# Kernel tuning notes

Hardware: AMD Instinct MI355X
Metric: run time of the kernel (lower is better)

## Reference

```python
import jax, jax.numpy as jnp
import numpy as np

B, H, W = 1, 32, 32
C, G, K = 128, 4, 15
GC = C // G          # group channels = 32
K2 = K * K           # 225
RED = 4              # SE reduction
KHID = 32            # kernel_net hidden


def setup_inputs() -> dict:
    key = jax.random.key(0)
    ks = jax.random.split(key, 24)
    def n(k, shape, s=0.02):
        return jax.random.normal(k, shape, jnp.float32) * s
    inp = {
        'x': jax.random.normal(ks[0], (B, H, W, C), jnp.float32),
        # scalars (torch: raw_sigma init = softplus^{-1}(0.3), base_offset_scale = 0.1)
        'raw_sigma': jnp.asarray(float(np.log(np.expm1(0.3))), jnp.float32),
        'base_offset_scale': jnp.asarray(0.1, jnp.float32),
        # input/output projections
        'w_in': n(ks[1], (C, C)), 'b_in': jnp.zeros((C,), jnp.float32),
        'w_out': n(ks[2], (C, C)), 'b_out': jnp.zeros((C,), jnp.float32),
        # dw_conv: depthwise 3x3 (HWIO, I=1 per group) + pointwise 1x1
        'dw_k': n(ks[3], (3, 3, 1, C), 0.1), 'dw_b': jnp.zeros((C,), jnp.float32),
        'pw_w': n(ks[4], (C, C)), 'pw_b': jnp.zeros((C,), jnp.float32),
        # offset / mask nets (zero-init in torch; small random here to exercise gather)
        'off_w': n(ks[5], (C, G * K2 * 2), 0.01), 'off_b': n(ks[6], (G * K2 * 2,), 0.01),
        'msk_w': n(ks[7], (C, G * K2), 0.01), 'msk_b': n(ks[8], (G * K2,), 0.01),
        # kernel_net: 2 -> 32 -> 32 -> G*GC
        'k1_w': n(ks[9], (2, KHID), 0.3), 'k1_b': jnp.zeros((KHID,), jnp.float32),
        'k2_w': n(ks[10], (KHID, KHID), 0.2), 'k2_b': jnp.zeros((KHID,), jnp.float32),
        'k3_w': n(ks[11], (KHID, G * GC), 0.2), 'k3_b': jnp.zeros((G * GC,), jnp.float32),
        # SE block
        'se1_w': n(ks[12], (C, C // RED), 0.1), 'se1_b': jnp.zeros((C // RED,), jnp.float32),
        'se2_w': n(ks[13], (C // RED, C), 0.1), 'se2_b': jnp.zeros((C,), jnp.float32),
    }
    return inp


def reference(x, raw_sigma, base_offset_scale, w_in, b_in, w_out, b_out,
              dw_k, dw_b, pw_w, pw_b, off_w, off_b, msk_w, msk_b,
              k1_w, k1_b, k2_w, k2_b, k3_w, k3_b, se1_w, se1_b, se2_w, se2_b):
    # sigma (scalar path, biases=None)
    sigma = jnp.clip(jax.nn.softplus(raw_sigma), 0.001, 0.5)
    grid = jnp.linspace(-0.5, 0.5, K)

    x_proj = x @ w_in + b_in                                   # [B,H,W,C]

    # dw_conv: depthwise 3x3 -> SiLU -> 1x1
    y = jax.lax.conv_general_dilated(
        x, dw_k, (1, 1), 'SAME',
        dimension_numbers=('NHWC', 'HWIO', 'NHWC'),
        feature_group_count=C) + dw_b
    x_dw = jax.nn.silu(y) @ pw_w + pw_b                        # [B,H,W,C]

    # Gaussian envelope over kernel grid, normalized (scalar sigma -> shape [K,K])
    gh = grid[:, None]; gw = grid[None, :]
    env = jnp.exp(-(gh ** 2 + gw ** 2) / (2.0 * sigma ** 2))
    env = env / jnp.clip(env.sum(), 1e-8)                      # [K,K]

    # dynamic kernel weights from grid positions (*2); replicate torch's
    # contiguous view (K,K,G,gc) -> (G,K2,gc)
    pos = jnp.stack(jnp.meshgrid(grid, grid, indexing='ij'), -1).reshape(K2, 2) * 2.0
    h1 = jax.nn.silu(pos @ k1_w + k1_b)
    h2 = jax.nn.silu(h1 @ k2_w + k2_b)
    kw = (h2 @ k3_w + k3_b).reshape(K, K, G, GC).reshape(G, K2, GC)  # [G,K2,gc]

    offsets = (x_dw @ off_w + off_b).reshape(B, H, W, G, K2, 2) * base_offset_scale
    raw_mask = (x_dw @ msk_w + msk_b).reshape(B, H, W, G, K2) * env.reshape(1, 1, 1, 1, K2)
    attn = jnp.nan_to_num(jax.nn.softmax(raw_mask, axis=-1))   # [B,H,W,G,K2]

    # reference sampling grid (integer offsets -K//2..K//2)
    ref = jnp.linspace(-(K // 2), K // 2, K)
    ref_grid = jnp.stack(jnp.meshgrid(ref, ref, indexing='ij'), -1).reshape(K2, 2)
    pos_h = jnp.arange(H, dtype=jnp.float32).reshape(1, H, 1, 1, 1)
    pos_w = jnp.arange(W, dtype=jnp.float32).reshape(1, 1, W, 1, 1)

    abs_h = pos_h + ref_grid[:, 0].reshape(1, 1, 1, 1, K2) + offsets[..., 0]
    abs_w = pos_w + ref_grid[:, 1].reshape(1, 1, 1, 1, K2) + offsets[..., 1]
    ah = jnp.clip(abs_h, 0.0, H - 1); aw = jnp.clip(abs_w, 0.0, W - 1)
    hf = jnp.clip(ah.astype(jnp.int32), 0, H - 1)
    wf = jnp.clip(aw.astype(jnp.int32), 0, W - 1)
    hc = jnp.clip(hf + 1, 0, H - 1)
    wc = jnp.clip(wf + 1, 0, W - 1)
    hw = ah - hf.astype(jnp.float32)
    ww = aw - wf.astype(jnp.float32)
    valid = (~((abs_h < 0) | (abs_h > H - 1) | (abs_w < 0) | (abs_w > W - 1))).astype(jnp.float32)

    x_g = x_proj.reshape(B, H, W, G, GC)
    b_idx = jnp.arange(B).reshape(B, 1, 1, 1, 1)
    g_idx = jnp.arange(G).reshape(1, 1, 1, G, 1)
    def gather(hi, wi):
        return x_g[b_idx, hi, wi, g_idx]                       # [B,H,W,G,K2,gc]

    sampled = (gather(hf, wf) * ((1 - hw) * (1 - ww) * valid)[..., None]
             + gather(hf, wc) * ((1 - hw) * ww * valid)[..., None]
             + gather(hc, wf) * (hw * (1 - ww) * valid)[..., None]
             + gather(hc, wc) * (hw * ww * valid)[..., None])

    sampled = sampled * kw.reshape(1, 1, 1, G, K2, GC)
    out = jnp.einsum('bhwgkc,bhwgk->bhwgc', sampled, attn).reshape(B, H, W, C)

    # SE block (mask=None, bias=None)
    pooled = out.mean(axis=(1, 2), keepdims=True)
    scale = jax.nn.sigmoid(jax.nn.silu(pooled @ se1_w + se1_b) @ se2_w + se2_b)
    out = out * scale

    return out @ w_out + b_out
```

## Files before the change

kernel.cpp:

```cpp
#include <hip/hip_runtime.h>
#include <math.h>

constexpr int H = 32, W = 32, C = 128, G = 4, K = 15, K2 = 225, GC = 32;
constexpr int NPIX = H * W;
constexpr int NOFF = G * K2 * 2;
constexpr int NMSK = G * K2;
constexpr int NTOT = NOFF + NMSK;
constexpr int KHID = 32;

constexpr size_t WS_ENV    = 0;
constexpr size_t WS_KW     = 256;
constexpr size_t WS_SCALE  = 29184;
constexpr size_t WS_PART   = 29312;
constexpr size_t WS_XPROJ  = 33792;
constexpr size_t WS_XDW    = 164864;
constexpr size_t WS_OUTPRE = 295936;
constexpr size_t WS_OFFS   = 427008;
constexpr size_t WS_MASK   = 2270208;

__device__ __forceinline__ float sigmoidf_(float v) { return 1.f / (1.f + expf(-v)); }
__device__ __forceinline__ float siluf_(float v)    { return v / (1.f + expf(-v)); }

__global__ void env_kernel(const float* __restrict__ raw_sigma, float* __restrict__ ws) {
    __shared__ float red[256];
    int tid = threadIdx.x;
    float xs = raw_sigma[0];
    float sp = fmaxf(xs, 0.f) + log1pf(expf(-fabsf(xs)));
    float sigma = fminf(fmaxf(sp, 0.001f), 0.5f);
    float inv2s2 = 1.f / (2.f * sigma * sigma);
    int i = tid / 15, j = tid % 15;
    float e = 0.f;
    if (tid < K2) {
        float gi = -0.5f + (float)i * (1.f / 14.f);
        float gj = -0.5f + (float)j * (1.f / 14.f);
        e = expf(-(gi * gi + gj * gj) * inv2s2);
    }
    red[tid] = e;
    __syncthreads();
    for (int s = 128; s > 0; s >>= 1) {
        if (tid < s) red[tid] += red[tid + s];
        __syncthreads();
    }
    float esum = fmaxf(red[0], 1e-8f);
    if (tid < K2) ws[WS_ENV + tid] = e / esum;
}

__global__ void kwmlp_kernel(const float* __restrict__ k1_w, const float* __restrict__ k1_b,
                             const float* __restrict__ k2_w, const float* __restrict__ k2_b,
                             const float* __restrict__ k3_w, const float* __restrict__ k3_b,
                             float* __restrict__ ws) {
    int k2i = blockIdx.x;
    int t = threadIdx.x;
    int i = k2i / 15, j = k2i % 15;
    float ph = (-0.5f + (float)i * (1.f / 14.f)) * 2.f;
    float pw = (-0.5f + (float)j * (1.f / 14.f)) * 2.f;
    __shared__ float h1[KHID], h2[KHID];
    if (t < KHID) {
        float a = fmaf(ph, k1_w[t], fmaf(pw, k1_w[KHID + t], k1_b[t]));
        h1[t] = siluf_(a);
    }
    __syncthreads();
    if (t < KHID) {
        float a = k2_b[t];
#pragma unroll
        for (int q = 0; q < KHID; q++) a = fmaf(h1[q], k2_w[q * KHID + t], a);
        h2[t] = siluf_(a);
    }
    __syncthreads();
    float a = k3_b[t];
#pragma unroll
    for (int q = 0; q < KHID; q++) a = fmaf(h2[q], k3_w[q * C + t], a);
    ws[WS_KW + (size_t)k2i * C + t] = a;
}

__global__ void front_kernel(const float* __restrict__ x,
                             const float* __restrict__ w_in, const float* __restrict__ b_in,
                             const float* __restrict__ dw_k, const float* __restrict__ dw_b,
                             const float* __restrict__ pw_w, const float* __restrict__ pw_b,
                             float* __restrict__ ws) {
    int p = blockIdx.x;
    int h = p >> 5, w = p & 31;
    int c = threadIdx.x;
    __shared__ float xs[C], ts[C];
    xs[c] = x[(size_t)p * C + c];
    float y = dw_b[c];
#pragma unroll
    for (int dy = 0; dy < 3; dy++) {
        int hh = h + dy - 1;
        if (hh < 0 || hh >= H) continue;
#pragma unroll
        for (int dx = 0; dx < 3; dx++) {
            int wq = w + dx - 1;
            if (wq < 0 || wq >= W) continue;
            y = fmaf(x[((size_t)hh * W + wq) * C + c], dw_k[(dy * 3 + dx) * C + c], y);
        }
    }
    ts[c] = siluf_(y);
    __syncthreads();
    float accp = b_in[c], accd = pw_b[c];
    for (int i = 0; i < C; i += 4) {
        float4 xv = *(const float4*)&xs[i];
        float4 tv = *(const float4*)&ts[i];
        accp = fmaf(xv.x, w_in[(size_t)(i + 0) * C + c], accp);
        accp = fmaf(xv.y, w_in[(size_t)(i + 1) * C + c], accp);
        accp = fmaf(xv.z, w_in[(size_t)(i + 2) * C + c], accp);
        accp = fmaf(xv.w, w_in[(size_t)(i + 3) * C + c], accp);
        accd = fmaf(tv.x, pw_w[(size_t)(i + 0) * C + c], accd);
        accd = fmaf(tv.y, pw_w[(size_t)(i + 1) * C + c], accd);
        accd = fmaf(tv.z, pw_w[(size_t)(i + 2) * C + c], accd);
        accd = fmaf(tv.w, pw_w[(size_t)(i + 3) * C + c], accd);
    }
    ws[WS_XPROJ + (size_t)p * C + c] = accp;
    ws[WS_XDW  + (size_t)p * C + c] = accd;
}

__global__ __launch_bounds__(256) void offmsk_gemm(const float* __restrict__ A,
                                                   const float* __restrict__ off_w,
                                                   const float* __restrict__ off_b,
                                                   const float* __restrict__ msk_w,
                                                   const float* __restrict__ msk_b,
                                                   const float* __restrict__ bos,
                                                   const float* __restrict__ env,
                                                   float* __restrict__ offs_out,
                                                   float* __restrict__ mask_out) {
    __shared__ float At[32][72];
    __shared__ float Bs[32][128];
    int tid = threadIdx.x;
    int c0 = blockIdx.x * 128;
    int p0 = blockIdx.y * 64;
    int tx = tid & 15, ty = tid >> 4;

    float acc[4][8];
#pragma unroll
    for (int i = 0; i < 4; i++)
#pragma unroll
        for (int j = 0; j < 8; j++) acc[i][j] = 0.f;

    int cB = c0 + (tid & 31) * 4;
    int kB = tid >> 5;
    bool bvalid = cB < NTOT;
    const float* bptr = nullptr;
    int bstride = 0;
    if (cB < NOFF)       { bptr = off_w + cB;          bstride = NOFF; }
    else if (bvalid)     { bptr = msk_w + (cB - NOFF); bstride = NMSK; }
    int rA = tid >> 3, k4A = (tid & 7) * 4;

    for (int kt = 0; kt < C; kt += 32) {
        if (kt) __syncthreads();
#pragma unroll
        for (int pass = 0; pass < 2; pass++) {
            int r = rA + pass * 32;
            float4 v = *(const float4*)&A[(size_t)(p0 + r) * C + kt + k4A];
            At[k4A + 0][r] = v.x; At[k4A + 1][r] = v.y;
            At[k4A + 2][r] = v.z; At[k4A + 3][r] = v.w;
        }
#pragma unroll
        for (int pass = 0; pass < 4; pass++) {
            int k = kB + pass * 8;
            float4 v = make_float4(0.f, 0.f, 0.f, 0.f);
            if (bvalid) v = *(const float4*)&bptr[(size_t)(kt + k) * bstride];
            *(float4*)&Bs[k][(tid & 31) * 4] = v;
        }
        __syncthreads();
#pragma unroll 8
        for (int k = 0; k < 32; k++) {
            const float4 a4 = *(const float4*)&At[k][ty * 4];
            const float4 b0 = *(const float4*)&Bs[k][tx * 8];
            const float4 b1 = *(const float4*)&Bs[k][tx * 8 + 4];
            const float av[4] = {a4.x, a4.y, a4.z, a4.w};
            const float bv[8] = {b0.x, b0.y, b0.z, b0.w, b1.x, b1.y, b1.z, b1.w};
#pragma unroll
            for (int i = 0; i < 4; i++)
#pragma unroll
                for (int j = 0; j < 8; j++)
                    acc[i][j] = fmaf(av[i], bv[j], acc[i][j]);
        }
    }

    int colbase = c0 + tx * 8;
    if (colbase >= NTOT) return;
    float bias[8], sc[8];
    float* obase;
    int ostride;
    bool full = (colbase + 8) <= NTOT;
    if (colbase < NOFF) {
        float s = bos[0];
#pragma unroll
        for (int j = 0; j < 8; j++) { bias[j] = off_b[colbase + j]; sc[j] = s; }
        obase = offs_out + colbase; ostride = NOFF;
    } else {
        int m0 = colbase - NOFF;
#pragma unroll
        for (int j = 0; j < 8; j++) {
            if (colbase + j < NTOT) { bias[j] = msk_b[m0 + j]; sc[j] = env[(m0 + j) % K2]; }
            else                    { bias[j] = 0.f; sc[j] = 0.f; }
        }
        obase = mask_out + m0; ostride = NMSK;
    }
#pragma unroll
    for (int i = 0; i < 4; i++) {
        size_t row = (size_t)(p0 + ty * 4 + i);
        if (full) {
            float4 r0 = make_float4((acc[i][0] + bias[0]) * sc[0], (acc[i][1] + bias[1]) * sc[1],
                                    (acc[i][2] + bias[2]) * sc[2], (acc[i][3] + bias[3]) * sc[3]);
            float4 r1 = make_float4((acc[i][4] + bias[4]) * sc[4], (acc[i][5] + bias[5]) * sc[5],
                                    (acc[i][6] + bias[6]) * sc[6], (acc[i][7] + bias[7]) * sc[7]);
            *(float4*)&obase[row * ostride]     = r0;
            *(float4*)&obase[row * ostride + 4] = r1;
        } else {
#pragma unroll
            for (int j = 0; j < 8; j++)
                if (colbase + j < NTOT)
                    obase[row * ostride + j] = (acc[i][j] + bias[j]) * sc[j];
        }
    }
}

__global__ __launch_bounds__(256) void sampler_kernel(const float* __restrict__ ws_offs,
                                                      const float* __restrict__ ws_mask,
                                                      const float* __restrict__ xproj,
                                                      const float* __restrict__ kwf,
                                                      float* __restrict__ outpre) {
    int p = blockIdx.x;
    int h = p >> 5, w = p & 31;
    int tid = threadIdx.x;

    __shared__ float  attn[NMSK];
    __shared__ float4 wgt4[NMSK];
    __shared__ int4   loc4[NMSK];
    __shared__ float4 psum4[256];

    {
        int lane = tid & 63;
        int g = tid >> 6;
        const float* mrow = ws_mask + (size_t)p * NMSK + g * K2;
        float v[4], ex[4];
        float mx = -1e30f;
#pragma unroll
        for (int q = 0; q < 4; q++) {
            int k = lane + q * 64;
            v[q] = (k < K2) ? mrow[k] : -1e30f;
            mx = fmaxf(mx, v[q]);
        }
#pragma unroll
        for (int s = 32; s > 0; s >>= 1) mx = fmaxf(mx, __shfl_xor(mx, s));
        float sum = 0.f;
#pragma unroll
        for (int q = 0; q < 4; q++) {
            int k = lane + q * 64;
            ex[q] = (k < K2) ? expf(v[q] - mx) : 0.f;
            sum += ex[q];
        }
#pragma unroll
        for (int s = 32; s > 0; s >>= 1) sum += __shfl_xor(sum, s);
        float inv = 1.f / sum;
#pragma unroll
        for (int q = 0; q < 4; q++) {
            int k = lane + q * 64;
            if (k < K2) attn[g * K2 + k] = ex[q] * inv;
        }
    }
    __syncthreads();

    for (int idx = tid; idx < NMSK; idx += 256) {
        int k = idx % K2;
        float2 o = *(const float2*)&ws_offs[(size_t)p * NOFF + idx * 2];
        float abs_h = (float)(h + k / 15 - 7) + o.x;
        float abs_w = (float)(w + k % 15 - 7) + o.y;
        float validf = (abs_h < 0.f || abs_h > 31.f || abs_w < 0.f || abs_w > 31.f) ? 0.f : 1.f;
        float ah = fminf(fmaxf(abs_h, 0.f), 31.f);
        float aw = fminf(fmaxf(abs_w, 0.f), 31.f);
        int hf = (int)ah, wf = (int)aw;
        int hc = min(hf + 1, 31), wc = min(wf + 1, 31);
        float hwt = ah - (float)hf, wwt = aw - (float)wf;
        float a = attn[idx] * validf;
        float u0 = 1.f - hwt, u1 = 1.f - wwt;
        wgt4[idx] = make_float4(a * u0 * u1, a * u0 * wwt, a * hwt * u1, a * hwt * wwt);
        loc4[idx] = make_int4((hf * W + wf) * C, (hf * W + wc) * C,
                              (hc * W + wf) * C, (hc * W + wc) * C);
    }
    __syncthreads();

    {
        int g  = tid >> 6;
        int s  = (tid >> 3) & 7;
        int cq = (tid & 7) * 4;
        const float* xpg = xproj + g * GC + cq;
        const float* kwg = kwf + (size_t)g * (K2 * GC) + cq;
        float4 acc = make_float4(0.f, 0.f, 0.f, 0.f);
        int k0 = s * 28;
        int k1 = (s == 7) ? K2 : k0 + 28;
        for (int k = k0; k < k1; k++) {
            int idx = g * K2 + k;
            int4   A  = loc4[idx];
            float4 Wv = wgt4[idx];
            float4 x00 = *(const float4*)(xpg + A.x);
            float4 x01 = *(const float4*)(xpg + A.y);
            float4 x10 = *(const float4*)(xpg + A.z);
            float4 x11 = *(const float4*)(xpg + A.w);
            float4 kw4 = *(const float4*)(kwg + k * GC);
            float sx = fmaf(Wv.w, x11.x, fmaf(Wv.z, x10.x, fmaf(Wv.y, x01.x, Wv.x * x00.x)));
            float sy = fmaf(Wv.w, x11.y, fmaf(Wv.z, x10.y, fmaf(Wv.y, x01.y, Wv.x * x00.y)));
            float sz = fmaf(Wv.w, x11.z, fmaf(Wv.z, x10.z, fmaf(Wv.y, x01.z, Wv.x * x00.z)));
            float sw = fmaf(Wv.w, x11.w, fmaf(Wv.z, x10.w, fmaf(Wv.y, x01.w, Wv.x * x00.w)));
            acc.x = fmaf(kw4.x, sx, acc.x);
            acc.y = fmaf(kw4.y, sy, acc.y);
            acc.z = fmaf(kw4.z, sz, acc.z);
            acc.w = fmaf(kw4.w, sw, acc.w);
        }
        psum4[tid] = acc;
    }
    __syncthreads();
    if (((tid >> 3) & 7) == 0) {
        int g = tid >> 6, cq = (tid & 7) * 4;
        float4 r = psum4[tid];
#pragma unroll
        for (int ss = 1; ss < 8; ss++) {
            float4 q = psum4[tid + ss * 8];
            r.x += q.x; r.y += q.y; r.z += q.z; r.w += q.w;
        }
        *(float4*)&outpre[(size_t)p * C + g * GC + cq] = r;
    }
}

__global__ void reduce1_kernel(const float* __restrict__ outpre, float* __restrict__ part) {
    int b = blockIdx.x;
    int c = threadIdx.x;
    float s = 0.f;
    for (int q = 0; q < 32; q++) s += outpre[(size_t)(b * 32 + q) * C + c];
    part[(size_t)b * C + c] = s;
}

__global__ void se_kernel(const float* __restrict__ part,
                          const float* __restrict__ se1_w, const float* __restrict__ se1_b,
                          const float* __restrict__ se2_w, const float* __restrict__ se2_b,
                          float* __restrict__ scale_out) {
    __shared__ float pooled[C];
    __shared__ float hid[KHID];
    int tid = threadIdx.x;
    float s = 0.f;
    for (int b = 0; b < 32; b++) s += part[(size_t)b * C + tid];
    pooled[tid] = s * (1.f / 1024.f);
    __syncthreads();
    if (tid < KHID) {
        float a = se1_b[tid];
        for (int cc = 0; cc < C; cc++) a = fmaf(pooled[cc], se1_w[cc * KHID + tid], a);
        hid[tid] = siluf_(a);
    }
    __syncthreads();
    float a = se2_b[tid];
#pragma unroll
    for (int q = 0; q < KHID; q++) a = fmaf(hid[q], se2_w[q * C + tid], a);
    scale_out[tid] = sigmoidf_(a);
}

__global__ void final_kernel(const float* __restrict__ outpre, const float* __restrict__ scale,
                             const float* __restrict__ w_out, const float* __restrict__ b_out,
                             float* __restrict__ out) {
    int p = blockIdx.x;
    int c = threadIdx.x;
    __shared__ float v[C];
    v[c] = outpre[(size_t)p * C + c] * scale[c];
    __syncthreads();
    float acc = b_out[c];
    for (int i = 0; i < C; i += 4) {
        float4 vv = *(const float4*)&v[i];
        acc = fmaf(vv.x, w_out[(size_t)(i + 0) * C + c], acc);
        acc = fmaf(vv.y, w_out[(size_t)(i + 1) * C + c], acc);
        acc = fmaf(vv.z, w_out[(size_t)(i + 2) * C + c], acc);
        acc = fmaf(vv.w, w_out[(size_t)(i + 3) * C + c], acc);
    }
    out[(size_t)p * C + c] = acc;
}

extern "C" void kernel_launch(void* const* d_in, const int* in_sizes, int n_in,
                              void* d_out, int out_size, void* d_ws, size_t ws_size,
                              hipStream_t stream) {
    const float* x         = (const float*)d_in[0];
    const float* raw_sigma = (const float*)d_in[1];
    const float* bos       = (const float*)d_in[2];
    const float* w_in      = (const float*)d_in[3];
    const float* b_in      = (const float*)d_in[4];
    const float* w_out     = (const float*)d_in[5];
    const float* b_out     = (const float*)d_in[6];
    const float* dw_k      = (const float*)d_in[7];
    const float* dw_b      = (const float*)d_in[8];
    const float* pw_w      = (const float*)d_in[9];
    const float* pw_b      = (const float*)d_in[10];
    const float* off_w     = (const float*)d_in[11];
    const float* off_b     = (const float*)d_in[12];
    const float* msk_w     = (const float*)d_in[13];
    const float* msk_b     = (const float*)d_in[14];
    const float* k1_w      = (const float*)d_in[15];
    const float* k1_b      = (const float*)d_in[16];
    const float* k2_w      = (const float*)d_in[17];
    const float* k2_b      = (const float*)d_in[18];
    const float* k3_w      = (const float*)d_in[19];
    const float* k3_b      = (const float*)d_in[20];
    const float* se1_w     = (const float*)d_in[21];
    const float* se1_b     = (const float*)d_in[22];
    const float* se2_w     = (const float*)d_in[23];
    const float* se2_b     = (const float*)d_in[24];

    float* ws  = (float*)d_ws;
    float* out = (float*)d_out;

    env_kernel<<<1, 256, 0, stream>>>(raw_sigma, ws);
    kwmlp_kernel<<<K2, C, 0, stream>>>(k1_w, k1_b, k2_w, k2_b, k3_w, k3_b, ws);
    front_kernel<<<NPIX, C, 0, stream>>>(x, w_in, b_in, dw_k, dw_b, pw_w, pw_b, ws);

    dim3 gg((NTOT + 127) / 128, NPIX / 64);
    offmsk_gemm<<<gg, 256, 0, stream>>>(ws + WS_XDW, off_w, off_b, msk_w, msk_b, bos,
                                        ws + WS_ENV, ws + WS_OFFS, ws + WS_MASK);

    sampler_kernel<<<NPIX, 256, 0, stream>>>(ws + WS_OFFS, ws + WS_MASK, ws + WS_XPROJ,
                                             ws + WS_KW, ws + WS_OUTPRE);

    reduce1_kernel<<<32, C, 0, stream>>>(ws + WS_OUTPRE, ws + WS_PART);
    se_kernel<<<1, C, 0, stream>>>(ws + WS_PART, se1_w, se1_b, se2_w, se2_b, ws + WS_SCALE);
    final_kernel<<<NPIX, C, 0, stream>>>(ws + WS_OUTPRE, ws + WS_SCALE, w_out, b_out, out);
}
```

Measured before the change: 78.68 us.

## Merge prep kernels, batch pixels per block, shrink GEMM tile, compact sampler

Merges the envelope and kernel-MLP launches into one prep kernel where each thread computes the whole MLP for a point. The front and final kernels now handle four pixels per 256-thread block, so each weight load is reused across two pixels. The offset/mask GEMM tile narrows to 64 columns, which gives more blocks and removes the partial-tile branch. The sampler handles two pixels per block, stores gather indices as ushort4, and reduces partial sums with shuffles instead of shared memory. Doing several unrelated changes at once makes it hard to attribute any effect, and the serial per-thread MLP could be slow.

Result: slower. 81.26 us (+3.3%).

```diff
diff --git a/kernel.cpp b/kernel.cpp
--- a/kernel.cpp
+++ b/kernel.cpp
@@ -21,97 +21,117 @@
 __device__ __forceinline__ float sigmoidf_(float v) { return 1.f / (1.f + expf(-v)); }
 __device__ __forceinline__ float siluf_(float v)    { return v / (1.f + expf(-v)); }
 
-__global__ void env_kernel(const float* __restrict__ raw_sigma, float* __restrict__ ws) {
-    __shared__ float red[256];
-    int tid = threadIdx.x;
-    float xs = raw_sigma[0];
-    float sp = fmaxf(xs, 0.f) + log1pf(expf(-fabsf(xs)));
-    float sigma = fminf(fmaxf(sp, 0.001f), 0.5f);
-    float inv2s2 = 1.f / (2.f * sigma * sigma);
-    int i = tid / 15, j = tid % 15;
-    float e = 0.f;
-    if (tid < K2) {
-        float gi = -0.5f + (float)i * (1.f / 14.f);
-        float gj = -0.5f + (float)j * (1.f / 14.f);
-        e = expf(-(gi * gi + gj * gj) * inv2s2);
-    }
-    red[tid] = e;
-    __syncthreads();
-    for (int s = 128; s > 0; s >>= 1) {
-        if (tid < s) red[tid] += red[tid + s];
-        __syncthreads();
-    }
-    float esum = fmaxf(red[0], 1e-8f);
-    if (tid < K2) ws[WS_ENV + tid] = e / esum;
-}
-
-__global__ void kwmlp_kernel(const float* __restrict__ k1_w, const float* __restrict__ k1_b,
+__device__ __forceinline__ void mlp_point(int k2i, int lane,
+                                          const float* __restrict__ k1_w, const float* __restrict__ k1_b,
+                                          const float* __restrict__ k2_w, const float* __restrict__ k2_b,
+                                          const float* __restrict__ k3_w, const float* __restrict__ k3_b,
+                                          float* __restrict__ ws) {
+    int i = k2i / 15, j = k2i % 15;
+    float ph = (-0.5f + (float)i * (1.f / 14.f)) * 2.f;
+    float pw = (-0.5f + (float)j * (1.f / 14.f)) * 2.f;
+    float h1[KHID], h2[KHID];
+#pragma unroll
+    for (int m = 0; m < KHID; m++)
+        h1[m] = siluf_(fmaf(ph, k1_w[m], fmaf(pw, k1_w[KHID + m], k1_b[m])));
+#pragma unroll
+    for (int m = 0; m < KHID; m++) {
+        float a = k2_b[m];
+#pragma unroll
+        for (int q = 0; q < KHID; q++) a = fmaf(h1[q], k2_w[q * KHID + m], a);
+        h2[m] = siluf_(a);
+    }
+#pragma unroll
+    for (int t = 0; t < 2; t++) {
+        int col = lane + t * 64;
+        float a = k3_b[col];
+#pragma unroll
+        for (int q = 0; q < KHID; q++) a = fmaf(h2[q], k3_w[q * C + col], a);
+        ws[WS_KW + (size_t)k2i * C + col] = a;
+    }
+}
+
+__global__ __launch_bounds__(256) void prep_kernel(const float* __restrict__ raw_sigma,
+                             const float* __restrict__ k1_w, const float* __restrict__ k1_b,
                              const float* __restrict__ k2_w, const float* __restrict__ k2_b,
                              const float* __restrict__ k3_w, const float* __restrict__ k3_b,
                              float* __restrict__ ws) {
-    int k2i = blockIdx.x;
-    int t = threadIdx.x;
-    int i = k2i / 15, j = k2i % 15;
-    float ph = (-0.5f + (float)i * (1.f / 14.f)) * 2.f;
-    float pw = (-0.5f + (float)j * (1.f / 14.f)) * 2.f;
-    __shared__ float h1[KHID], h2[KHID];
-    if (t < KHID) {
-        float a = fmaf(ph, k1_w[t], fmaf(pw, k1_w[KHID + t], k1_b[t]));
-        h1[t] = siluf_(a);
-    }
-    __syncthreads();
-    if (t < KHID) {
-        float a = k2_b[t];
-#pragma unroll
-        for (int q = 0; q < KHID; q++) a = fmaf(h1[q], k2_w[q * KHID + t], a);
-        h2[t] = siluf_(a);
-    }
-    __syncthreads();
-    float a = k3_b[t];
-#pragma unroll
-    for (int q = 0; q < KHID; q++) a = fmaf(h2[q], k3_w[q * C + t], a);
-    ws[WS_KW + (size_t)k2i * C + t] = a;
-}
-
-__global__ void front_kernel(const float* __restrict__ x,
+    int tid = threadIdx.x;
+    if (blockIdx.x == 0) {
+        __shared__ float red[256];
+        float xs = raw_sigma[0];
+        float sp = fmaxf(xs, 0.f) + log1pf(expf(-fabsf(xs)));
+        float sigma = fminf(fmaxf(sp, 0.001f), 0.5f);
+        float inv2s2 = 1.f / (2.f * sigma * sigma);
+        int i = tid / 15, j = tid % 15;
+        float e = 0.f;
+        if (tid < K2) {
+            float gi = -0.5f + (float)i * (1.f / 14.f);
+            float gj = -0.5f + (float)j * (1.f / 14.f);
+            e = expf(-(gi * gi + gj * gj) * inv2s2);
+        }
+        red[tid] = e;
+        __syncthreads();
+        for (int s = 128; s > 0; s >>= 1) {
+            if (tid < s) red[tid] += red[tid + s];
+            __syncthreads();
+        }
+        float esum = fmaxf(red[0], 1e-8f);
+        if (tid < K2) ws[WS_ENV + tid] = e / esum;
+        if (tid < 64) mlp_point(224, tid, k1_w, k1_b, k2_w, k2_b, k3_w, k3_b, ws);
+    } else {
+        int k2i = (blockIdx.x - 1) * 4 + (tid >> 6);
+        mlp_point(k2i, tid & 63, k1_w, k1_b, k2_w, k2_b, k3_w, k3_b, ws);
+    }
+}
+
+__global__ __launch_bounds__(256) void front_kernel(const float* __restrict__ x,
                              const float* __restrict__ w_in, const float* __restrict__ b_in,
                              const float* __restrict__ dw_k, const float* __restrict__ dw_b,
                              const float* __restrict__ pw_w, const float* __restrict__ pw_b,
                              float* __restrict__ ws) {
-    int p = blockIdx.x;
-    int h = p >> 5, w = p & 31;
-    int c = threadIdx.x;
-    __shared__ float xs[C], ts[C];
-    xs[c] = x[(size_t)p * C + c];
-    float y = dw_b[c];
-#pragma unroll
-    for (int dy = 0; dy < 3; dy++) {
-        int hh = h + dy - 1;
-        if (hh < 0 || hh >= H) continue;
-#pragma unroll
-        for (int dx = 0; dx < 3; dx++) {
-            int wq = w + dx - 1;
-            if (wq < 0 || wq >= W) continue;
-            y = fmaf(x[((size_t)hh * W + wq) * C + c], dw_k[(dy * 3 + dx) * C + c], y);
-        }
-    }
-    ts[c] = siluf_(y);
-    __syncthreads();
-    float accp = b_in[c], accd = pw_b[c];
+    int p0 = blockIdx.x * 4;
+    int tid = threadIdx.x;
+    int c = tid & 127;
+    int pp = tid >> 7;
+    __shared__ float xs[4][C], ts[4][C];
+#pragma unroll
+    for (int q = 0; q < 2; q++) {
+        int px = pp * 2 + q;
+        int p = p0 + px;
+        int h = p >> 5, w = p & 31;
+        xs[px][c] = x[(size_t)p * C + c];
+        float y = dw_b[c];
+#pragma unroll
+        for (int dy = 0; dy < 3; dy++) {
+            int hh = h + dy - 1;
+            if (hh < 0 || hh >= H) continue;
+#pragma unroll
+            for (int dx = 0; dx < 3; dx++) {
+                int wq = w + dx - 1;
+                if (wq < 0 || wq >= W) continue;
+                y = fmaf(x[((size_t)hh * W + wq) * C + c], dw_k[(dy * 3 + dx) * C + c], y);
+            }
+        }
+        ts[px][c] = siluf_(y);
+    }
+    __syncthreads();
+    float ap0 = b_in[c], ap1 = b_in[c], ad0 = pw_b[c], ad1 = pw_b[c];
+    int b0 = pp * 2, b1 = pp * 2 + 1;
     for (int i = 0; i < C; i += 4) {
-        float4 xv = *(const float4*)&xs[i];
-        float4 tv = *(const float4*)&ts[i];
-        accp = fmaf(xv.x, w_in[(size_t)(i + 0) * C + c], accp);
-        accp = fmaf(xv.y, w_in[(size_t)(i + 1) * C + c], accp);
-        accp = fmaf(xv.z, w_in[(size_t)(i + 2) * C + c], accp);
-        accp = fmaf(xv.w, w_in[(size_t)(i + 3) * C + c], accp);
-        accd = fmaf(tv.x, pw_w[(size_t)(i + 0) * C + c], accd);
-        accd = fmaf(tv.y, pw_w[(size_t)(i + 1) * C + c], accd);
-        accd = fmaf(tv.z, pw_w[(size_t)(i + 2) * C + c], accd);
-        accd = fmaf(tv.w, pw_w[(size_t)(i + 3) * C + c], accd);
-    }
-    ws[WS_XPROJ + (size_t)p * C + c] = accp;
-    ws[WS_XDW  + (size_t)p * C + c] = accd;
+#pragma unroll
+        for (int u = 0; u < 4; u++) {
+            float wi = w_in[(size_t)(i + u) * C + c];
+            float pi = pw_w[(size_t)(i + u) * C + c];
+            ap0 = fmaf(xs[b0][i + u], wi, ap0);
+            ap1 = fmaf(xs[b1][i + u], wi, ap1);
+            ad0 = fmaf(ts[b0][i + u], pi, ad0);
+            ad1 = fmaf(ts[b1][i + u], pi, ad1);
+        }
+    }
+    ws[WS_XPROJ + (size_t)(p0 + b0) * C + c] = ap0;
+    ws[WS_XPROJ + (size_t)(p0 + b1) * C + c] = ap1;
+    ws[WS_XDW  + (size_t)(p0 + b0) * C + c] = ad0;
+    ws[WS_XDW  + (size_t)(p0 + b1) * C + c] = ad1;
 }
 
 __global__ __launch_bounds__(256) void offmsk_gemm(const float* __restrict__ A,
@@ -124,25 +144,24 @@
                                                    float* __restrict__ offs_out,
                                                    float* __restrict__ mask_out) {
     __shared__ float At[32][72];
-    __shared__ float Bs[32][128];
-    int tid = threadIdx.x;
-    int c0 = blockIdx.x * 128;
+    __shared__ float Bs[32][64];
+    int tid = threadIdx.x;
+    int c0 = blockIdx.x * 64;
     int p0 = blockIdx.y * 64;
     int tx = tid & 15, ty = tid >> 4;
 
-    float acc[4][8];
+    float acc[4][4];
 #pragma unroll
     for (int i = 0; i < 4; i++)
 #pragma unroll
-        for (int j = 0; j < 8; j++) acc[i][j] = 0.f;
-
-    int cB = c0 + (tid & 31) * 4;
-    int kB = tid >> 5;
-    bool bvalid = cB < NTOT;
-    const float* bptr = nullptr;
-    int bstride = 0;
+        for (int j = 0; j < 4; j++) acc[i][j] = 0.f;
+
+    int cL = (tid * 4) & 63;
+    int kL = (tid * 4) >> 6;
+    int cB = c0 + cL;
+    const float* bptr = nullptr; int bstride = 0;
     if (cB < NOFF)       { bptr = off_w + cB;          bstride = NOFF; }
-    else if (bvalid)     { bptr = msk_w + (cB - NOFF); bstride = NMSK; }
+    else if (cB < NTOT)  { bptr = msk_w + (cB - NOFF); bstride = NMSK; }
     int rA = tid >> 3, k4A = (tid & 7) * 4;
 
     for (int kt = 0; kt < C; kt += 32) {
@@ -153,66 +172,48 @@
             float4 v = *(const float4*)&A[(size_t)(p0 + r) * C + kt + k4A];
             At[k4A + 0][r] = v.x; At[k4A + 1][r] = v.y;
             At[k4A + 2][r] = v.z; At[k4A + 3][r] = v.w;
-        }
-#pragma unroll
-        for (int pass = 0; pass < 4; pass++) {
-            int k = kB + pass * 8;
-            float4 v = make_float4(0.f, 0.f, 0.f, 0.f);
-            if (bvalid) v = *(const float4*)&bptr[(size_t)(kt + k) * bstride];
-            *(float4*)&Bs[k][(tid & 31) * 4] = v;
+            int k = kL + pass * 16;
+            float4 bv = make_float4(0.f, 0.f, 0.f, 0.f);
+            if (bptr) bv = *(const float4*)&bptr[(size_t)(kt + k) * bstride];
+            *(float4*)&Bs[k][cL] = bv;
         }
         __syncthreads();
-#pragma unroll 8
+#pragma unroll
         for (int k = 0; k < 32; k++) {
-            const float4 a4 = *(const float4*)&At[k][ty * 4];
-            const float4 b0 = *(const float4*)&Bs[k][tx * 8];
-            const float4 b1 = *(const float4*)&Bs[k][tx * 8 + 4];
+            float4 a4 = *(const float4*)&At[k][ty * 4];
+            float4 b4 = *(const float4*)&Bs[k][tx * 4];
             const float av[4] = {a4.x, a4.y, a4.z, a4.w};
-            const float bv[8] = {b0.x, b0.y, b0.z, b0.w, b1.x, b1.y, b1.z, b1.w};
+            const float bv[4] = {b4.x, b4.y, b4.z, b4.w};
 #pragma unroll
             for (int i = 0; i < 4; i++)
 #pragma unroll
-                for (int j = 0; j < 8; j++)
+                for (int j = 0; j < 4; j++)
                     acc[i][j] = fmaf(av[i], bv[j], acc[i][j]);
         }
     }
 
-    int colbase = c0 + tx * 8;
+    int colbase = c0 + tx * 4;
     if (colbase >= NTOT) return;
-    float bias[8], sc[8];
+    float bias[4], sc[4];
     float* obase;
     int ostride;
-    bool full = (colbase + 8) <= NTOT;
     if (colbase < NOFF) {
         float s = bos[0];
 #pragma unroll
-        for (int j = 0; j < 8; j++) { bias[j] = off_b[colbase + j]; sc[j] = s; }
+        for (int j = 0; j < 4; j++) { bias[j] = off_b[colbase + j]; sc[j] = s; }
         obase = offs_out + colbase; ostride = NOFF;
     } else {
         int m0 = colbase - NOFF;
 #pragma unroll
-        for (int j = 0; j < 8; j++) {
-            if (colbase + j < NTOT) { bias[j] = msk_b[m0 + j]; sc[j] = env[(m0 + j) % K2]; }
-            else                    { bias[j] = 0.f; sc[j] = 0.f; }
-        }
+        for (int j = 0; j < 4; j++) { bias[j] = msk_b[m0 + j]; sc[j] = env[(m0 + j) % K2]; }
         obase = mask_out + m0; ostride = NMSK;
     }
 #pragma unroll
     for (int i = 0; i < 4; i++) {
         size_t row = (size_t)(p0 + ty * 4 + i);
-        if (full) {
-            float4 r0 = make_float4((acc[i][0] + bias[0]) * sc[0], (acc[i][1] + bias[1]) * sc[1],
-                                    (acc[i][2] + bias[2]) * sc[2], (acc[i][3] + bias[3]) * sc[3]);
-            float4 r1 = make_float4((acc[i][4] + bias[4]) * sc[4], (acc[i][5] + bias[5]) * sc[5],
-                                    (acc[i][6] + bias[6]) * sc[6], (acc[i][7] + bias[7]) * sc[7]);
-            *(float4*)&obase[row * ostride]     = r0;
-            *(float4*)&obase[row * ostride + 4] = r1;
-        } else {
-#pragma unroll
-            for (int j = 0; j < 8; j++)
-                if (colbase + j < NTOT)
-                    obase[row * ostride + j] = (acc[i][j] + bias[j]) * sc[j];
-        }
+        float4 r0 = make_float4((acc[i][0] + bias[0]) * sc[0], (acc[i][1] + bias[1]) * sc[1],
+                                (acc[i][2] + bias[2]) * sc[2], (acc[i][3] + bias[3]) * sc[3]);
+        *(float4*)&obase[row * ostride] = r0;
     }
 }
 
@@ -221,50 +222,55 @@
                                                       const float* __restrict__ xproj,
                                                       const float* __restrict__ kwf,
                                                       float* __restrict__ outpre) {
-    int p = blockIdx.x;
-    int h = p >> 5, w = p & 31;
-    int tid = threadIdx.x;
-
-    __shared__ float  attn[NMSK];
-    __shared__ float4 wgt4[NMSK];
-    __shared__ int4   loc4[NMSK];
-    __shared__ float4 psum4[256];
+    int p0 = blockIdx.x * 2;
+    int h = p0 >> 5;
+    int tid = threadIdx.x;
+
+    __shared__ float   attn_s[2][NMSK];
+    __shared__ float4  wgt_s[2][NMSK];
+    __shared__ ushort4 loc_s[2][NMSK];
 
     {
-        int lane = tid & 63;
-        int g = tid >> 6;
-        const float* mrow = ws_mask + (size_t)p * NMSK + g * K2;
-        float v[4], ex[4];
+        int half = tid >> 5;
+        int l32 = tid & 31;
+        int px = half >> 2, g = half & 3;
+        const float* mrow = ws_mask + (size_t)(p0 + px) * NMSK + g * K2;
+        float v[8];
         float mx = -1e30f;
 #pragma unroll
-        for (int q = 0; q < 4; q++) {
-            int k = lane + q * 64;
+        for (int q = 0; q < 8; q++) {
+            int k = l32 + q * 32;
             v[q] = (k < K2) ? mrow[k] : -1e30f;
             mx = fmaxf(mx, v[q]);
         }
 #pragma unroll
-        for (int s = 32; s > 0; s >>= 1) mx = fmaxf(mx, __shfl_xor(mx, s));
+        for (int s = 16; s > 0; s >>= 1) mx = fmaxf(mx, __shfl_xor(mx, s));
         float sum = 0.f;
 #pragma unroll
-        for (int q = 0; q < 4; q++) {
-            int k = lane + q * 64;
-            ex[q] = (k < K2) ? expf(v[q] - mx) : 0.f;
-            sum += ex[q];
-        }
-#pragma unroll
-        for (int s = 32; s > 0; s >>= 1) sum += __shfl_xor(sum, s);
+        for (int q = 0; q < 8; q++) {
+            int k = l32 + q * 32;
+            v[q] = (k < K2) ? expf(v[q] - mx) : 0.f;
+            sum += v[q];
+        }
+#pragma unroll
+        for (int s = 16; s > 0; s >>= 1) sum += __shfl_xor(sum, s);
         float inv = 1.f / sum;
 #pragma unroll
-        for (int q = 0; q < 4; q++) {
-            int k = lane + q * 64;
-            if (k < K2) attn[g * K2 + k] = ex[q] * inv;
-        }
-    }
-    __syncthreads();
-
-    for (int idx = tid; idx < NMSK; idx += 256) {
-        int k = idx % K2;
-        float2 o = *(const float2*)&ws_offs[(size_t)p * NOFF + idx * 2];
+        for (int q = 0; q < 8; q++) {
+            int k = l32 + q * 32;
+            if (k < K2) attn_s[px][g * K2 + k] = v[q] * inv;
+        }
+    }
+    __syncthreads();
+
+    for (int e = tid; e < 2 * NMSK; e += 256) {
+        int px = (e >= NMSK) ? 1 : 0;
+        int m = e - px * NMSK;
+        int g = m / K2;
+        int k = m - g * K2;
+        int p = p0 + px;
+        int w = p & 31;
+        float2 o = *(const float2*)&ws_offs[(size_t)p * NOFF + m * 2];
         float abs_h = (float)(h + k / 15 - 7) + o.x;
         float abs_w = (float)(w + k % 15 - 7) + o.y;
         float validf = (abs_h < 0.f || abs_h > 31.f || abs_w < 0.f || abs_w > 31.f) ? 0.f : 1.f;
@@ -273,31 +279,32 @@
         int hf = (int)ah, wf = (int)aw;
         int hc = min(hf + 1, 31), wc = min(wf + 1, 31);
         float hwt = ah - (float)hf, wwt = aw - (float)wf;
-        float a = attn[idx] * validf;
+        float a = attn_s[px][m] * validf;
         float u0 = 1.f - hwt, u1 = 1.f - wwt;
-        wgt4[idx] = make_float4(a * u0 * u1, a * u0 * wwt, a * hwt * u1, a * hwt * wwt);
-        loc4[idx] = make_int4((hf * W + wf) * C, (hf * W + wc) * C,
-                              (hc * W + wf) * C, (hc * W + wc) * C);
+        wgt_s[px][m] = make_float4(a * u0 * u1, a * u0 * wwt, a * hwt * u1, a * hwt * wwt);
+        loc_s[px][m] = make_ushort4((unsigned short)(hf * W + wf), (unsigned short)(hf * W + wc),
+                                    (unsigned short)(hc * W + wf), (unsigned short)(hc * W + wc));
     }
     __syncthreads();
 
     {
-        int g  = tid >> 6;
-        int s  = (tid >> 3) & 7;
-        int cq = (tid & 7) * 4;
-        const float* xpg = xproj + g * GC + cq;
-        const float* kwg = kwf + (size_t)g * (K2 * GC) + cq;
+        int cq = tid & 7;
+        int s  = (tid >> 3) & 3;
+        int g  = (tid >> 5) & 3;
+        int px = tid >> 7;
+        int k0 = (s * K2) >> 2;
+        int k1 = ((s + 1) * K2) >> 2;
+        const float* xpg = xproj + g * GC + cq * 4;
+        const float* kwg = kwf + (size_t)g * (K2 * GC) + cq * 4;
         float4 acc = make_float4(0.f, 0.f, 0.f, 0.f);
-        int k0 = s * 28;
-        int k1 = (s == 7) ? K2 : k0 + 28;
         for (int k = k0; k < k1; k++) {
-            int idx = g * K2 + k;
-            int4   A  = loc4[idx];
-            float4 Wv = wgt4[idx];
-            float4 x00 = *(const float4*)(xpg + A.x);
-            float4 x01 = *(const float4*)(xpg + A.y);
-            float4 x10 = *(const float4*)(xpg + A.z);
-            float4 x11 = *(const float4*)(xpg + A.w);
+            int m = g * K2 + k;
+            ushort4 L  = loc_s[px][m];
+            float4  Wv = wgt_s[px][m];
+            float4 x00 = *(const float4*)(xpg + (int)L.x * C);
+            float4 x01 = *(const float4*)(xpg + (int)L.y * C);
+            float4 x10 = *(const float4*)(xpg + (int)L.z * C);
+            float4 x11 = *(const float4*)(xpg + (int)L.w * C);
             float4 kw4 = *(const float4*)(kwg + k * GC);
             float sx = fmaf(Wv.w, x11.x, fmaf(Wv.z, x10.x, fmaf(Wv.y, x01.x, Wv.x * x00.x)));
             float sy = fmaf(Wv.w, x11.y, fmaf(Wv.z, x10.y, fmaf(Wv.y, x01.y, Wv.x * x00.y)));
@@ -308,18 +315,12 @@
             acc.z = fmaf(kw4.z, sz, acc.z);
             acc.w = fmaf(kw4.w, sw, acc.w);
         }
-        psum4[tid] = acc;
-    }
-    __syncthreads();
-    if (((tid >> 3) & 7) == 0) {
-        int g = tid >> 6, cq = (tid & 7) * 4;
-        float4 r = psum4[tid];
-#pragma unroll
-        for (int ss = 1; ss < 8; ss++) {
-            float4 q = psum4[tid + ss * 8];
-            r.x += q.x; r.y += q.y; r.z += q.z; r.w += q.w;
-        }
-        *(float4*)&outpre[(size_t)p * C + g * GC + cq] = r;
+        acc.x += __shfl_xor(acc.x, 8);  acc.y += __shfl_xor(acc.y, 8);
+        acc.z += __shfl_xor(acc.z, 8);  acc.w += __shfl_xor(acc.w, 8);
+        acc.x += __shfl_xor(acc.x, 16); acc.y += __shfl_xor(acc.y, 16);
+        acc.z += __shfl_xor(acc.z, 16); acc.w += __shfl_xor(acc.w, 16);
+        if (s == 0)
+            *(float4*)&outpre[(size_t)(p0 + px) * C + g * GC + cq * 4] = acc;
     }
 }
 
@@ -354,23 +355,34 @@
     scale_out[tid] = sigmoidf_(a);
 }
 
-__global__ void final_kernel(const float* __restrict__ outpre, const float* __restrict__ scale,
+__global__ __launch_bounds__(256) void final_kernel(const float* __restrict__ outpre,
+                             const float* __restrict__ scale,
                              const float* __restrict__ w_out, const float* __restrict__ b_out,
                              float* __restrict__ out) {
-    int p = blockIdx.x;
-    int c = threadIdx.x;
-    __shared__ float v[C];
-    v[c] = outpre[(size_t)p * C + c] * scale[c];
-    __syncthreads();
-    float acc = b_out[c];
+    int p0 = blockIdx.x * 4;
+    int tid = threadIdx.x;
+    int c = tid & 127;
+    int pp = tid >> 7;
+    __shared__ float v[4][C];
+    float scv = scale[c];
+#pragma unroll
+    for (int q = 0; q < 2; q++) {
+        int px = pp * 2 + q;
+        v[px][c] = outpre[(size_t)(p0 + px) * C + c] * scv;
+    }
+    __syncthreads();
+    float a0 = b_out[c], a1 = b_out[c];
+    int b0 = pp * 2, b1 = pp * 2 + 1;
     for (int i = 0; i < C; i += 4) {
-        float4 vv = *(const float4*)&v[i];
-        acc = fmaf(vv.x, w_out[(size_t)(i + 0) * C + c], acc);
-        acc = fmaf(vv.y, w_out[(size_t)(i + 1) * C + c], acc);
-        acc = fmaf(vv.z, w_out[(size_t)(i + 2) * C + c], acc);
-        acc = fmaf(vv.w, w_out[(size_t)(i + 3) * C + c], acc);
-    }
-    out[(size_t)p * C + c] = acc;
+#pragma unroll
+        for (int u = 0; u < 4; u++) {
+            float wv = w_out[(size_t)(i + u) * C + c];
+            a0 = fmaf(v[b0][i + u], wv, a0);
+            a1 = fmaf(v[b1][i + u], wv, a1);
+        }
+    }
+    out[(size_t)(p0 + b0) * C + c] = a0;
+    out[(size_t)(p0 + b1) * C + c] = a1;
 }
 
 extern "C" void kernel_launch(void* const* d_in, const int* in_sizes, int n_in,
@@ -405,18 +417,17 @@
     float* ws  = (float*)d_ws;
     float* out = (float*)d_out;
 
-    env_kernel<<<1, 256, 0, stream>>>(raw_sigma, ws);
-    kwmlp_kernel<<<K2, C, 0, stream>>>(k1_w, k1_b, k2_w, k2_b, k3_w, k3_b, ws);
-    front_kernel<<<NPIX, C, 0, stream>>>(x, w_in, b_in, dw_k, dw_b, pw_w, pw_b, ws);
-
-    dim3 gg((NTOT + 127) / 128, NPIX / 64);
+    prep_kernel<<<57, 256, 0, stream>>>(raw_sigma, k1_w, k1_b, k2_w, k2_b, k3_w, k3_b, ws);
+    front_kernel<<<NPIX / 4, 256, 0, stream>>>(x, w_in, b_in, dw_k, dw_b, pw_w, pw_b, ws);
+
+    dim3 gg((NTOT + 63) / 64, NPIX / 64);
     offmsk_gemm<<<gg, 256, 0, stream>>>(ws + WS_XDW, off_w, off_b, msk_w, msk_b, bos,
                                         ws + WS_ENV, ws + WS_OFFS, ws + WS_MASK);
 
-    sampler_kernel<<<NPIX, 256, 0, stream>>>(ws + WS_OFFS, ws + WS_MASK, ws + WS_XPROJ,
-                                             ws + WS_KW, ws + WS_OUTPRE);
+    sampler_kernel<<<NPIX / 2, 256, 0, stream>>>(ws + WS_OFFS, ws + WS_MASK, ws + WS_XPROJ,
+                                                 ws + WS_KW, ws + WS_OUTPRE);
 
     reduce1_kernel<<<32, C, 0, stream>>>(ws + WS_OUTPRE, ws + WS_PART);
     se_kernel<<<1, C, 0, stream>>>(ws + WS_PART, se1_w, se1_b, se2_w, se2_b, ws + WS_SCALE);
-    final_kernel<<<NPIX, C, 0, stream>>>(ws + WS_OUTPRE, ws + WS_SCALE, w_out, b_out, out);
-}
+    final_kernel<<<NPIX / 4, 256, 0, stream>>>(ws + WS_OUTPRE, ws + WS_SCALE, w_out, b_out, out);
+}
```
